# Performance work log

Measured on AMD Instinct MI355X. Metric: run time of the kernel, lower is better.

Reference implementation:

```python
import jax, jax.numpy as jnp
import numpy as np

EPS = 1e-6
BASE_THETA = 10000.0


def setup_inputs() -> dict:
    key = jax.random.key(0)
    ks = jax.random.split(key, 6)
    S, E = 4096, 4096
    scale = 1.0 / np.sqrt(E)
    return {
        "x": jax.random.normal(ks[0], (S, E), dtype=jnp.float32),
        "w_q": jax.random.normal(ks[1], (E, E), dtype=jnp.float32) * scale,
        "w_k": jax.random.normal(ks[2], (E, E), dtype=jnp.float32) * scale,
        "w_v": jax.random.normal(ks[3], (E, E), dtype=jnp.float32) * scale,
        "w_out": jax.random.normal(ks[4], (E, E), dtype=jnp.float32) * scale,
        "scaling_factor": jax.random.uniform(ks[5], (E,), dtype=jnp.float32, minval=0.5, maxval=1.5),
    }


def _rope_apply(t, cos, sin):
    # t: (S, D) fp16; cos/sin: (S, D//2) fp16. Closed form of the per-position
    # block-diagonal 2x2 rotation matrix matmul in the original loop:
    # out[2j]   =  t[2j]*cos + t[2j+1]*sin
    # out[2j+1] = -t[2j]*sin + t[2j+1]*cos
    S, D = t.shape
    t2 = t.reshape(S, D // 2, 2)
    even, odd = t2[..., 0], t2[..., 1]
    out = jnp.stack([even * cos + odd * sin, -even * sin + odd * cos], axis=-1)
    return out.reshape(S, D)


def reference(x, w_q, w_k, w_v, w_out, scaling_factor):
    f16, f32 = jnp.float16, jnp.float32
    S, E = x.shape
    # __init__: q / q_inv / head rotations are identity; quantize = cast fp16 (scale 1).
    # q_inv * scaling_factor.view(1,-1) == diag(scaling_factor) -> row-scale weights.
    wq = (scaling_factor[:, None] * w_q).astype(f16)
    wk = (scaling_factor[:, None] * w_k).astype(f16)
    wv = (scaling_factor[:, None] * w_v).astype(f16)
    wo = w_out.astype(f16)

    # input @ identity; rms_norm in fp32
    xn = x * jax.lax.rsqrt(jnp.mean(x * x, axis=-1, keepdims=True) + EPS)
    xq = xn.astype(f16)

    # quantized matmuls: fp16 operands, fp32 accumulation, cast back to fp16
    q = (xq.astype(f32) @ wq.astype(f32)).astype(f16)
    k = (xq.astype(f32) @ wk.astype(f32)).astype(f16)
    v = (xq.astype(f32) @ wv.astype(f32)).astype(f16)

    # RoPE over full feature dim (size = E), vectorized over positions
    pos = jnp.arange(S, dtype=f32)[:, None]
    j = jnp.arange(E // 2, dtype=f32)[None, :]
    theta = pos / jnp.power(BASE_THETA, 2.0 * j / E)
    cos = jnp.cos(theta).astype(f16)
    sin = jnp.sin(theta).astype(f16)
    q = _rope_apply(q, cos, sin)
    k = _rope_apply(k, cos, sin)

    # rot_head_k_tiled is identity -> quantize is just fp16 cast (already fp16)
    scores = (q.astype(f32) @ k.T.astype(f32)).astype(f16)
    scores = scores / np.float16(np.sqrt(E))
    # causal mask: strict upper triangle -> -inf
    row = jnp.arange(S)[:, None]
    col = jnp.arange(S)[None, :]
    scores = jnp.where(col > row, jnp.float16(-jnp.inf), scores)
    attn_w = jax.nn.softmax(scores, axis=1)
    attn = attn_w @ v  # fp16 matmul as in original

    out = (attn.astype(f32) @ wo.astype(f32)).astype(f16)
    return out
```

## Files before the change

kernel.cpp:

```cpp
#include <hip/hip_runtime.h>
#include <hip/hip_bf16.h>
#include <cmath>


typedef _Float16 f16;
typedef _Float16 f16x4 __attribute__((ext_vector_type(4)));
typedef _Float16 f16x8 __attribute__((ext_vector_type(8)));
typedef float f32x4 __attribute__((ext_vector_type(4)));

#define S_DIM 4096
#define E_DIM 4096

__device__ __forceinline__ void gload_lds16(const void* g, void* l) {
  __builtin_amdgcn_global_load_lds((const __attribute__((address_space(1))) void*)g,
                                   (__attribute__((address_space(3))) void*)l,
                                   16, 0, 0);
}

__global__ __launch_bounds__(256) void rmsnorm_f16(const float* __restrict__ x,
                                                   f16* __restrict__ xq, int E) {
  const int row = blockIdx.x;
  const int t = threadIdx.x;
  const float4* xr = (const float4*)(x + (size_t)row * E);
  float4 v[4];
  float ss = 0.f;
#pragma unroll
  for (int i = 0; i < 4; ++i) {
    v[i] = xr[t + 256 * i];
    ss += v[i].x * v[i].x + v[i].y * v[i].y + v[i].z * v[i].z + v[i].w * v[i].w;
  }
#pragma unroll
  for (int o = 1; o < 64; o <<= 1) ss += __shfl_xor(ss, o);
  __shared__ float red[4];
  const int wid = t >> 6, lane = t & 63;
  if (lane == 0) red[wid] = ss;
  __syncthreads();
  const float tot = red[0] + red[1] + red[2] + red[3];
  const float r = 1.0f / sqrtf(tot / (float)E + 1e-6f);
  f16* xo = xq + (size_t)row * E;
#pragma unroll
  for (int i = 0; i < 4; ++i) {
    f16x4 o;
    o[0] = (f16)(v[i].x * r);
    o[1] = (f16)(v[i].y * r);
    o[2] = (f16)(v[i].z * r);
    o[3] = (f16)(v[i].w * r);
    *(f16x4*)(xo + 4 * (t + 256 * i)) = o;
  }
}

__global__ __launch_bounds__(256) void wconv_t(const float* __restrict__ W,
                                               const float* __restrict__ s,
                                               f16* __restrict__ WT, int N) {
  __shared__ f16 tile[64][65];
  const int tr = blockIdx.y * 64;
  const int tc = blockIdx.x * 64;
  const int t = threadIdx.x;
  const int r = t / 16;
  const int c4 = (t % 16) * 4;
#pragma unroll
  for (int i = 0; i < 4; ++i) {
    const int row = r + i * 16;
    float4 w = *(const float4*)(W + (size_t)(tr + row) * N + tc + c4);
    const float sc = s ? s[tr + row] : 1.0f;
    tile[row][c4 + 0] = (f16)(w.x * sc);
    tile[row][c4 + 1] = (f16)(w.y * sc);
    tile[row][c4 + 2] = (f16)(w.z * sc);
    tile[row][c4 + 3] = (f16)(w.w * sc);
  }
  __syncthreads();
#pragma unroll
  for (int i = 0; i < 4; ++i) {
    const int row = r + i * 16;
    f16x4 o;
    o[0] = tile[c4 + 0][row];
    o[1] = tile[c4 + 1][row];
    o[2] = tile[c4 + 2][row];
    o[3] = tile[c4 + 3][row];
    *(f16x4*)(WT + (size_t)(tc + row) * N + tr + c4) = o;
  }
}

__global__ __launch_bounds__(256) void transpose_f16(const f16* __restrict__ V,
                                                     f16* __restrict__ VT,
                                                     int R, int C) {
  __shared__ f16 tile[64][65];
  const int tr = blockIdx.y * 64;
  const int tc = blockIdx.x * 64;
  const int t = threadIdx.x;
  const int r = t / 16;
  const int c4 = (t % 16) * 4;
#pragma unroll
  for (int i = 0; i < 4; ++i) {
    const int row = r + i * 16;
    f16x4 in = *(const f16x4*)(V + (size_t)(tr + row) * C + tc + c4);
    tile[row][c4 + 0] = in[0];
    tile[row][c4 + 1] = in[1];
    tile[row][c4 + 2] = in[2];
    tile[row][c4 + 3] = in[3];
  }
  __syncthreads();
#pragma unroll
  for (int i = 0; i < 4; ++i) {
    const int row = r + i * 16;
    f16x4 o;
    o[0] = tile[c4 + 0][row];
    o[1] = tile[c4 + 1][row];
    o[2] = tile[c4 + 2][row];
    o[3] = tile[c4 + 3][row];
    *(f16x4*)(VT + (size_t)(tc + row) * R + tr + c4) = o;
  }
}

__global__ __launch_bounds__(256) void freq_tab_k(float* __restrict__ tab) {
  const int j = blockIdx.x * 256 + threadIdx.x;
  if (j < 2048) tab[j] = (float)pow(10000.0, (double)j / 2048.0);
}

__global__ __launch_bounds__(256) void rope_qk(f16* __restrict__ q,
                                               f16* __restrict__ k,
                                               const float* __restrict__ ftab,
                                               int E) {
  const int idx = blockIdx.x * 256 + threadIdx.x;
  const int cpr = E / 8;
  const int pos = idx / cpr;
  const int ch = idx % cpr;
  const int j0 = ch * 4;
  const float fpos = (float)pos;
  f16x8 qv = *(f16x8*)(q + (size_t)idx * 8);
  f16x8 kv = *(f16x8*)(k + (size_t)idx * 8);
  f16x8 qo, ko;
#pragma unroll
  for (int p = 0; p < 4; ++p) {
    const int j = j0 + p;
    const float th = fpos / ftab[j];
    float sn, cs;
    sincosf(th, &sn, &cs);
    const f16 c16 = (f16)cs, s16 = (f16)sn;
    const float c = (float)c16, s = (float)s16;
    {
      const float e = (float)qv[2 * p], o = (float)qv[2 * p + 1];
      const f16 t1 = (f16)(e * c), t2 = (f16)(o * s);
      const f16 u1 = (f16)(-(e * s)), u2 = (f16)(o * c);
      qo[2 * p] = (f16)((float)t1 + (float)t2);
      qo[2 * p + 1] = (f16)((float)u1 + (float)u2);
    }
    {
      const float e = (float)kv[2 * p], o = (float)kv[2 * p + 1];
      const f16 t1 = (f16)(e * c), t2 = (f16)(o * s);
      const f16 u1 = (f16)(-(e * s)), u2 = (f16)(o * c);
      ko[2 * p] = (f16)((float)t1 + (float)t2);
      ko[2 * p + 1] = (f16)((float)u1 + (float)u2);
    }
  }
  *(f16x8*)(q + (size_t)idx * 8) = qo;
  *(f16x8*)(k + (size_t)idx * 8) = ko;
}

__global__ __launch_bounds__(256) void softmax_causal(f16* __restrict__ sc, int S) {
  const int row = blockIdx.x;
  const int t = threadIdx.x;
  f16* p = sc + (size_t)row * S;
  float v[16];
  bool msk[16];
#pragma unroll
  for (int i = 0; i < 2; ++i) {
    f16x8 a = *(const f16x8*)(p + (size_t)(i * 256 + t) * 8);
#pragma unroll
    for (int j = 0; j < 8; ++j) v[i * 8 + j] = (float)a[j];
  }
  float m = -1e30f;
#pragma unroll
  for (int i = 0; i < 2; ++i)
#pragma unroll
    for (int j = 0; j < 8; ++j) {
      const int col = (i * 256 + t) * 8 + j;
      const int ii = i * 8 + j;
      msk[ii] = (col > row);
      if (!msk[ii]) m = fmaxf(m, v[ii]);
    }
#pragma unroll
  for (int o = 1; o < 64; o <<= 1) m = fmaxf(m, __shfl_xor(m, o));
  __shared__ float red[4];
  const int wid = t >> 6, lane = t & 63;
  if (lane == 0) red[wid] = m;
  __syncthreads();
  m = fmaxf(fmaxf(red[0], red[1]), fmaxf(red[2], red[3]));
  __syncthreads();
  f16 e16[16];
  float sum = 0.f;
#pragma unroll
  for (int i = 0; i < 16; ++i) {
    if (msk[i]) {
      e16[i] = (f16)0.0f;
    } else {
      const f16 d16 = (f16)(v[i] - m);
      e16[i] = (f16)expf((float)d16);
      sum += (float)e16[i];
    }
  }
#pragma unroll
  for (int o = 1; o < 64; o <<= 1) sum += __shfl_xor(sum, o);
  if (lane == 0) red[wid] = sum;
  __syncthreads();
  sum = red[0] + red[1] + red[2] + red[3];
  const f16 den16 = (f16)sum;
  const float den = (float)den16;
#pragma unroll
  for (int i = 0; i < 2; ++i) {
    f16x8 o;
#pragma unroll
    for (int j = 0; j < 8; ++j) {
      const int ii = i * 8 + j;
      o[j] = msk[ii] ? (f16)0.0f : (f16)((float)e16[ii] / den);
    }
    *(f16x8*)(p + (size_t)(i * 256 + t) * 8) = o;
  }
}

__device__ __forceinline__ void store_out(f16* p, f16 v) { *p = v; }
__device__ __forceinline__ void store_out(float* p, f16 v) { *p = (float)v; }

template <typename OUT>
__global__ __launch_bounds__(512, 2) void gemm256(const f16* __restrict__ A,
                                                  const f16* __restrict__ BT,
                                                  OUT* __restrict__ C,
                                                  int M, int N, int K, float alpha,
                                                  int mode) {
  if (mode == 1 && blockIdx.x > blockIdx.y) return;
  const int bm = blockIdx.y * 256, bn = blockIdx.x * 256;
  const int kend = (mode == 2) ? (bm + 256 < K ? bm + 256 : K) : K;
  const int nt = kend >> 6;

  extern __shared__ char smem[];
  f16(*lds)[2][256][64] = (f16(*)[2][256][64])smem;

  const int tid = threadIdx.x;
  const int lane = tid & 63;
  const int wid = tid >> 6;
  const int wr = wid >> 2;
  const int wc = wid & 3;
  const f16* Ab = A + (size_t)bm * K;
  const f16* Bb = BT + (size_t)bn * K;

  const int l8 = lane >> 3;
  const int gxor8 = ((lane & 7) ^ l8) * 8;
  const int lr = lane & 15;
  const int shi = lane >> 4;
  const int rsw = lr & 7;

  auto STAGE_P = [&](int p) {
    const int c = p + 6;
    const int Ts = c >> 2, hh = c & 3;
    if (Ts >= nt) return;
    const int k0 = Ts << 6;
    const int bsel = Ts & 1;
#pragma unroll
    for (int l = 0; l < 2; ++l) {
      const int rih0 = wid * 16 + l * 8;
      if (hh == 0 || hh == 3) {
        const int row0 = (rih0 & 63) + ((rih0 >> 6) << 7) + ((hh == 3) ? 64 : 0);
        gload_lds16(Ab + (size_t)(row0 + l8) * K + k0 + gxor8,
                    &lds[bsel][0][row0][0]);
      } else {
        const int row0 = (rih0 & 31) + ((rih0 >> 5) << 6) + ((hh == 2) ? 32 : 0);
        gload_lds16(Bb + (size_t)(row0 + l8) * K + k0 + gxor8,
                    &lds[bsel][1][row0][0]);
      }
    }
  };

  f32x4 acc[8][4] = {};
  f16x8 afr0[4][2], afr1[4][2], b0r[2][2], b1r[2][2];

#pragma unroll
  for (int p = -6; p < 0; ++p) STAGE_P(p);

  for (int T = 0; T < nt; ++T) {
    const int cur = T & 1;
    __builtin_amdgcn_sched_barrier(0);
    if (T + 1 < nt) {
      asm volatile("s_waitcnt vmcnt(4)" ::: "memory");
    } else {
      asm volatile("s_waitcnt vmcnt(0)" ::: "memory");
    }
    __builtin_amdgcn_sched_barrier(0);
    __builtin_amdgcn_s_barrier();
    __builtin_amdgcn_sched_barrier(0);
#pragma unroll
    for (int m2 = 0; m2 < 4; ++m2)
#pragma unroll
      for (int kk = 0; kk < 2; ++kk)
        afr0[m2][kk] = *(const f16x8*)&lds[cur][0][wr * 128 + m2 * 16 + lr]
                                          [((kk * 4 + shi) ^ rsw) * 8];
#pragma unroll
    for (int n2 = 0; n2 < 2; ++n2)
#pragma unroll
      for (int kk = 0; kk < 2; ++kk)
        b0r[n2][kk] = *(const f16x8*)&lds[cur][1][wc * 64 + n2 * 16 + lr]
                                         [((kk * 4 + shi) ^ rsw) * 8];
    STAGE_P(4 * T);
    __builtin_amdgcn_sched_barrier(0);
    if (T > 0) {
      __builtin_amdgcn_s_setprio(1);
#pragma unroll
      for (int m2 = 0; m2 < 4; ++m2)
#pragma unroll
        for (int n2 = 0; n2 < 2; ++n2)
#pragma unroll
          for (int kk = 0; kk < 2; ++kk)
            acc[4 + m2][2 + n2] = __builtin_amdgcn_mfma_f32_16x16x32_f16(
                afr1[m2][kk], b1r[n2][kk], acc[4 + m2][2 + n2], 0, 0, 0);
      __builtin_amdgcn_s_setprio(0);
    }
    __builtin_amdgcn_sched_barrier(0);
#pragma unroll
    for (int n2 = 0; n2 < 2; ++n2)
#pragma unroll
      for (int kk = 0; kk < 2; ++kk)
        b1r[n2][kk] = *(const f16x8*)&lds[cur][1][wc * 64 + 32 + n2 * 16 + lr]
                                         [((kk * 4 + shi) ^ rsw) * 8];
    STAGE_P(4 * T + 1);
    __builtin_amdgcn_sched_barrier(0);
    __builtin_amdgcn_s_setprio(1);
#pragma unroll
    for (int m2 = 0; m2 < 4; ++m2)
#pragma unroll
      for (int n2 = 0; n2 < 2; ++n2)
#pragma unroll
        for (int kk = 0; kk < 2; ++kk)
          acc[m2][n2] = __builtin_amdgcn_mfma_f32_16x16x32_f16(
              afr0[m2][kk], b0r[n2][kk], acc[m2][n2], 0, 0, 0);
    __builtin_amdgcn_s_setprio(0);
    __builtin_amdgcn_sched_barrier(0);
    __builtin_amdgcn_s_barrier();
    __builtin_amdgcn_sched_barrier(0);
#pragma unroll
    for (int m2 = 0; m2 < 4; ++m2)
#pragma unroll
      for (int kk = 0; kk < 2; ++kk)
        afr1[m2][kk] = *(const f16x8*)&lds[cur][0][wr * 128 + 64 + m2 * 16 + lr]
                                          [((kk * 4 + shi) ^ rsw) * 8];
    STAGE_P(4 * T + 2);
    __builtin_amdgcn_sched_barrier(0);
    __builtin_amdgcn_s_setprio(1);
#pragma unroll
    for (int m2 = 0; m2 < 4; ++m2)
#pragma unroll
      for (int n2 = 0; n2 < 2; ++n2)
#pragma unroll
        for (int kk = 0; kk < 2; ++kk)
          acc[m2][2 + n2] = __builtin_amdgcn_mfma_f32_16x16x32_f16(
              afr0[m2][kk], b1r[n2][kk], acc[m2][2 + n2], 0, 0, 0);
    __builtin_amdgcn_s_setprio(0);
    __builtin_amdgcn_sched_barrier(0);
    STAGE_P(4 * T + 3);
    __builtin_amdgcn_sched_barrier(0);
    __builtin_amdgcn_s_setprio(1);
#pragma unroll
    for (int m2 = 0; m2 < 4; ++m2)
#pragma unroll
      for (int n2 = 0; n2 < 2; ++n2)
#pragma unroll
        for (int kk = 0; kk < 2; ++kk)
          acc[4 + m2][n2] = __builtin_amdgcn_mfma_f32_16x16x32_f16(
              afr1[m2][kk], b0r[n2][kk], acc[4 + m2][n2], 0, 0, 0);
    __builtin_amdgcn_s_setprio(0);
  }
  __builtin_amdgcn_s_setprio(1);
#pragma unroll
  for (int m2 = 0; m2 < 4; ++m2)
#pragma unroll
    for (int n2 = 0; n2 < 2; ++n2)
#pragma unroll
      for (int kk = 0; kk < 2; ++kk)
        acc[4 + m2][2 + n2] = __builtin_amdgcn_mfma_f32_16x16x32_f16(
            afr1[m2][kk], b1r[n2][kk], acc[4 + m2][2 + n2], 0, 0, 0);
  __builtin_amdgcn_s_setprio(0);

  const int rb = bm + wr * 128 + (lane >> 4) * 4;
  const int cb = bn + wc * 64 + (lane & 15);
#pragma unroll
  for (int mm = 0; mm < 8; ++mm)
#pragma unroll
    for (int nn = 0; nn < 4; ++nn) {
      const int col = cb + nn * 16;
#pragma unroll
      for (int r = 0; r < 4; ++r) {
        f16 h = (f16)acc[mm][nn][r];
        if (alpha != 1.0f) h = (f16)((float)h * alpha);
        store_out(&C[(size_t)(rb + mm * 16 + r) * N + col], h);
      }
    }
}

extern "C" void kernel_launch(void* const* d_in, const int* in_sizes, int n_in,
                              void* d_out, int out_size, void* d_ws, size_t ws_size,
                              hipStream_t stream) {
  const float* x = (const float*)d_in[0];
  const float* wq = (const float*)d_in[1];
  const float* wk = (const float*)d_in[2];
  const float* wv = (const float*)d_in[3];
  const float* wo = (const float*)d_in[4];
  const float* sf = (const float*)d_in[5];
  float* out = (float*)d_out;

  const int S = S_DIM, E = E_DIM;
  const size_t U = (size_t)S * E * sizeof(f16);
  char* ws = (char*)d_ws;
  f16* xq = (f16*)(ws + 0 * U);
  f16* wT = (f16*)(ws + 1 * U);
  f16* q  = (f16*)(ws + 2 * U);
  f16* k  = (f16*)(ws + 3 * U);
  f16* v  = (f16*)d_out;

  const int LDSB = 131072;
  hipFuncSetAttribute(reinterpret_cast<const void*>(&gemm256<f16>),
                      hipFuncAttributeMaxDynamicSharedMemorySize, LDSB);
  hipFuncSetAttribute(reinterpret_cast<const void*>(&gemm256<float>),
                      hipFuncAttributeMaxDynamicSharedMemorySize, LDSB);

  dim3 b256(256), b512(512);
  dim3 gT(E / 64, E / 64);
  dim3 gG(E / 256, S / 256);

  rmsnorm_f16<<<S, b256, 0, stream>>>(x, xq, E);

  wconv_t<<<gT, b256, 0, stream>>>(wq, sf, wT, E);
  gemm256<f16><<<gG, b512, LDSB, stream>>>(xq, wT, q, S, E, E, 1.0f, 0);
  wconv_t<<<gT, b256, 0, stream>>>(wk, sf, wT, E);
  gemm256<f16><<<gG, b512, LDSB, stream>>>(xq, wT, k, S, E, E, 1.0f, 0);
  wconv_t<<<gT, b256, 0, stream>>>(wv, sf, wT, E);
  gemm256<f16><<<gG, b512, LDSB, stream>>>(xq, wT, v, S, E, E, 1.0f, 0);

  float* ftab = (float*)wT;
  freq_tab_k<<<8, b256, 0, stream>>>(ftab);
  rope_qk<<<(S * (E / 8)) / 256, b256, 0, stream>>>(q, k, ftab, E);

  f16* sc = wT;
  gemm256<f16><<<dim3(S / 256, S / 256), b512, LDSB, stream>>>(q, k, sc, S, S, E,
                                                               1.0f / 64.0f, 1);
  softmax_causal<<<S, b256, 0, stream>>>(sc, S);

  f16* vT = xq;
  transpose_f16<<<dim3(E / 64, S / 64), b256, 0, stream>>>(v, vT, S, E);

  f16* attn = q;
  gemm256<f16><<<gG, b512, LDSB, stream>>>(sc, vT, attn, S, E, S, 1.0f, 2);

  f16* wT2 = k;
  wconv_t<<<gT, b256, 0, stream>>>(wo, (const float*)nullptr, wT2, E);
  gemm256<float><<<gG, b512, LDSB, stream>>>(attn, wT2, out, S, E, E, 1.0f, 0);
}
```

Baseline: 796.4 us.

## Fuse RoPE into Q/K GEMM epilogue and remap workgroups across XCDs

Removes the standalone rope_qk kernel and applies the rotary rotation in the Q and K projection GEMM epilogue, using a lane shuffle to fetch the paired column. The frequency table moves into an unused region of the output buffer. This saves a full read and write of q and k. All GEMMs also remap block IDs so that consecutive tiles are spread across the 8 XCDs, aiming for better L2 locality. The epilogue now calls sincosf per element, which adds ALU work, and the block remap changes the order in which tiles are scheduled.

```diff
diff --git a/kernel.cpp b/kernel.cpp
--- a/kernel.cpp
+++ b/kernel.cpp
@@ -117,46 +117,6 @@
   if (j < 2048) tab[j] = (float)pow(10000.0, (double)j / 2048.0);
 }
 
-__global__ __launch_bounds__(256) void rope_qk(f16* __restrict__ q,
-                                               f16* __restrict__ k,
-                                               const float* __restrict__ ftab,
-                                               int E) {
-  const int idx = blockIdx.x * 256 + threadIdx.x;
-  const int cpr = E / 8;
-  const int pos = idx / cpr;
-  const int ch = idx % cpr;
-  const int j0 = ch * 4;
-  const float fpos = (float)pos;
-  f16x8 qv = *(f16x8*)(q + (size_t)idx * 8);
-  f16x8 kv = *(f16x8*)(k + (size_t)idx * 8);
-  f16x8 qo, ko;
-#pragma unroll
-  for (int p = 0; p < 4; ++p) {
-    const int j = j0 + p;
-    const float th = fpos / ftab[j];
-    float sn, cs;
-    sincosf(th, &sn, &cs);
-    const f16 c16 = (f16)cs, s16 = (f16)sn;
-    const float c = (float)c16, s = (float)s16;
-    {
-      const float e = (float)qv[2 * p], o = (float)qv[2 * p + 1];
-      const f16 t1 = (f16)(e * c), t2 = (f16)(o * s);
-      const f16 u1 = (f16)(-(e * s)), u2 = (f16)(o * c);
-      qo[2 * p] = (f16)((float)t1 + (float)t2);
-      qo[2 * p + 1] = (f16)((float)u1 + (float)u2);
-    }
-    {
-      const float e = (float)kv[2 * p], o = (float)kv[2 * p + 1];
-      const f16 t1 = (f16)(e * c), t2 = (f16)(o * s);
-      const f16 u1 = (f16)(-(e * s)), u2 = (f16)(o * c);
-      ko[2 * p] = (f16)((float)t1 + (float)t2);
-      ko[2 * p + 1] = (f16)((float)u1 + (float)u2);
-    }
-  }
-  *(f16x8*)(q + (size_t)idx * 8) = qo;
-  *(f16x8*)(k + (size_t)idx * 8) = ko;
-}
-
 __global__ __launch_bounds__(256) void softmax_causal(f16* __restrict__ sc, int S) {
   const int row = blockIdx.x;
   const int t = threadIdx.x;
@@ -226,9 +186,18 @@
                                                   const f16* __restrict__ BT,
                                                   OUT* __restrict__ C,
                                                   int M, int N, int K, float alpha,
-                                                  int mode) {
-  if (mode == 1 && blockIdx.x > blockIdx.y) return;
-  const int bm = blockIdx.y * 256, bn = blockIdx.x * 256;
+                                                  int mode,
+                                                  const float* __restrict__ ftab) {
+  const int nwgx = gridDim.x;
+  const int nwg = nwgx * gridDim.y;
+  int bid = blockIdx.y * nwgx + blockIdx.x;
+  if ((nwg & 7) == 0) {
+    const int cpx = nwg >> 3;
+    bid = (bid & 7) * cpx + (bid >> 3);
+  }
+  const int bx = bid % nwgx, by = bid / nwgx;
+  if (mode == 1 && bx > by) return;
+  const int bm = by * 256, bn = bx * 256;
   const int kend = (mode == 2) ? (bm + 256 < K ? bm + 256 : K) : K;
   const int nt = kend >> 6;
 
@@ -385,10 +354,24 @@
 #pragma unroll
     for (int nn = 0; nn < 4; ++nn) {
       const int col = cb + nn * 16;
+      float freqv = 1.0f;
+      if (mode == 3) freqv = ftab[col >> 1];
 #pragma unroll
       for (int r = 0; r < 4; ++r) {
         f16 h = (f16)acc[mm][nn][r];
         if (alpha != 1.0f) h = (f16)((float)h * alpha);
+        if (mode == 3) {
+          const int row = rb + mm * 16 + r;
+          const float hf = (float)h;
+          const float other = __shfl_xor(hf, 1);
+          float sn, cs;
+          sincosf((float)row / freqv, &sn, &cs);
+          const float c = (float)(f16)cs, s = (float)(f16)sn;
+          if (col & 1)
+            h = (f16)((float)(f16)(-(other * s)) + (float)(f16)(hf * c));
+          else
+            h = (f16)((float)(f16)(hf * c) + (float)(f16)(other * s));
+        }
         store_out(&C[(size_t)(rb + mm * 16 + r) * N + col], h);
       }
     }
@@ -413,6 +396,7 @@
   f16* q  = (f16*)(ws + 2 * U);
   f16* k  = (f16*)(ws + 3 * U);
   f16* v  = (f16*)d_out;
+  float* ftab = out + 12 * 1024 * 1024;
 
   const int LDSB = 131072;
   hipFuncSetAttribute(reinterpret_cast<const void*>(&gemm256<f16>),
@@ -425,30 +409,28 @@
   dim3 gG(E / 256, S / 256);
 
   rmsnorm_f16<<<S, b256, 0, stream>>>(x, xq, E);
+  freq_tab_k<<<8, b256, 0, stream>>>(ftab);
 
   wconv_t<<<gT, b256, 0, stream>>>(wq, sf, wT, E);
-  gemm256<f16><<<gG, b512, LDSB, stream>>>(xq, wT, q, S, E, E, 1.0f, 0);
+  gemm256<f16><<<gG, b512, LDSB, stream>>>(xq, wT, q, S, E, E, 1.0f, 3, ftab);
   wconv_t<<<gT, b256, 0, stream>>>(wk, sf, wT, E);
-  gemm256<f16><<<gG, b512, LDSB, stream>>>(xq, wT, k, S, E, E, 1.0f, 0);
+  gemm256<f16><<<gG, b512, LDSB, stream>>>(xq, wT, k, S, E, E, 1.0f, 3, ftab);
   wconv_t<<<gT, b256, 0, stream>>>(wv, sf, wT, E);
-  gemm256<f16><<<gG, b512, LDSB, stream>>>(xq, wT, v, S, E, E, 1.0f, 0);
-
-  float* ftab = (float*)wT;
-  freq_tab_k<<<8, b256, 0, stream>>>(ftab);
-  rope_qk<<<(S * (E / 8)) / 256, b256, 0, stream>>>(q, k, ftab, E);
+  gemm256<f16><<<gG, b512, LDSB, stream>>>(xq, wT, v, S, E, E, 1.0f, 0, nullptr);
 
   f16* sc = wT;
-  gemm256<f16><<<dim3(S / 256, S / 256), b512, LDSB, stream>>>(q, k, sc, S, S, E,
-                                                               1.0f / 64.0f, 1);
+  gemm256<f16><<<dim3(S / 256, S / 256), b512, LDSB, stream>>>(
+      q, k, sc, S, S, E, 1.0f / 64.0f, 1, nullptr);
   softmax_causal<<<S, b256, 0, stream>>>(sc, S);
 
   f16* vT = xq;
   transpose_f16<<<dim3(E / 64, S / 64), b256, 0, stream>>>(v, vT, S, E);
 
   f16* attn = q;
-  gemm256<f16><<<gG, b512, LDSB, stream>>>(sc, vT, attn, S, E, S, 1.0f, 2);
+  gemm256<f16><<<gG, b512, LDSB, stream>>>(sc, vT, attn, S, E, S, 1.0f, 2, nullptr);
 
   f16* wT2 = k;
   wconv_t<<<gT, b256, 0, stream>>>(wo, (const float*)nullptr, wT2, E);
-  gemm256<float><<<gG, b512, LDSB, stream>>>(attn, wT2, out, S, E, E, 1.0f, 0);
-}
+  gemm256<float><<<gG, b512, LDSB, stream>>>(attn, wT2, out, S, E, E, 1.0f, 0,
+                                             nullptr);
+}
```

New measurement: 1.027 ms. 1.29x slower.
